# Kernel optimization log

Hardware: AMD Instinct MI355X
Metric: run time of the kernel (lower is better)

Reference implementation:

```python
import jax, jax.numpy as jnp
import numpy as np

B, N, DIN, H, D = 16, 1024, 128, 4, 32  # batch, n_agents, input_dim, heads, head_dim
NEG = -9e15


def setup_inputs() -> dict:
    key = jax.random.key(0)
    k1, k2, k3, k4 = jax.random.split(key, 4)
    x = jax.random.normal(k1, (B, N, DIN), jnp.float32)
    adj = jax.random.randint(k2, (B, N, N), 0, 2, jnp.int32)
    # params (xavier-ish scale)
    W = jax.random.normal(k3, (DIN, H * D), jnp.float32) * np.float32(1.0 / np.sqrt(DIN))
    b = jnp.zeros((H * D,), jnp.float32)
    a = jax.random.normal(k4, (2 * D, 1), jnp.float32) * np.float32(0.1)
    return {"x": x, "adj": adj, "W": W, "b": b, "a": a}


def reference(x, adj, W, b, a):
    Bb, Nn, _ = x.shape
    h = (x @ W + b).reshape(Bb, Nn, H, D)              # [B,N,H,D]
    # GAT trick: concat([h_i,h_j]) @ a == h_i@a[:D] + h_j@a[D:]
    a_i, a_j = a[:D, 0], a[D:, 0]
    e_i = jnp.einsum('bnhd,d->bnh', h, a_i)
    e_j = jnp.einsum('bnhd,d->bnh', h, a_j)
    e = e_i[:, :, None, :] + e_j[:, None, :, :]        # [B,N,N,H]
    e = jnp.where(e > 0, e, 0.2 * e)                   # LeakyReLU(0.2)
    e = jnp.where(adj[..., None] > 0, e, NEG)          # adjacency mask
    attn = jax.nn.softmax(e, axis=2)                   # softmax over neighbors j
    out = jnp.einsum('bijh,bjhd->bihd', attn, h)       # per-head aggregation
    return out.reshape(Bb, Nn, H * D)                  # concat heads
```

## Files before the change

kernel.cpp:

```cpp
#include <hip/hip_runtime.h>
#include <hip/hip_bf16.h>

#define Bdim 16
#define Ndim 1024
#define Hh   4
#define HDc  128
#define L2E  1.4426950408889634f

typedef float  float4v  __attribute__((ext_vector_type(4)));
typedef int    int4v    __attribute__((ext_vector_type(4)));
typedef short  short8   __attribute__((ext_vector_type(8)));
typedef unsigned short ushort4v __attribute__((ext_vector_type(4)));

__device__ __forceinline__ unsigned short bf16_rne(float f) {
    unsigned u = __float_as_uint(f);
    u = u + 0x7FFFu + ((u >> 16) & 1u);
    return (unsigned short)(u >> 16);
}

__device__ __forceinline__ void gl_lds16(const void* g, void* l) {
    __builtin_amdgcn_global_load_lds(
        (const __attribute__((address_space(1))) unsigned int*)g,
        (__attribute__((address_space(3))) unsigned int*)l, 16, 0, 0);
}

__global__ __launch_bounds__(256) void split_w_kernel(
    const float* __restrict__ W, const float* __restrict__ bias,
    const float* __restrict__ a,
    unsigned short* __restrict__ WTh, unsigned short* __restrict__ WTl,
    float* __restrict__ bias2)
{
    const int t = threadIdx.x, blk = blockIdx.x;
    if (blk < 16) {
        int r  = blk * 8 + (t >> 5);
        int k0 = (t & 31) * 4;
        #pragma unroll
        for (int j = 0; j < 4; ++j) {
            float f = W[(size_t)(k0 + j) * HDc + r];
            unsigned short hi = bf16_rne(f);
            WTh[r * 128 + k0 + j] = hi;
            WTl[r * 128 + k0 + j] = bf16_rne(f - __uint_as_float((unsigned)hi << 16));
        }
    } else {
        #pragma unroll
        for (int rep = 0; rep < 2; ++rep) {
            int task = t + rep * 256;
            int row = task >> 2, hh = task & 3;
            float si = 0.f, sj = 0.f;
            #pragma unroll
            for (int d4 = 0; d4 < 8; ++d4) {
                float4v wv = *(const float4v*)(W + (size_t)row * HDc + hh * 32 + d4 * 4);
                float4v av = *(const float4v*)(a + d4 * 4);
                float4v bv = *(const float4v*)(a + 32 + d4 * 4);
                #pragma unroll
                for (int kk = 0; kk < 4; ++kk) {
                    si = fmaf(wv[kk], av[kk], si);
                    sj = fmaf(wv[kk], bv[kk], sj);
                }
            }
            float vi = si * L2E, vj = sj * L2E;
            unsigned short hi = bf16_rne(vi);
            WTh[(128 + hh) * 128 + row] = hi;
            WTl[(128 + hh) * 128 + row] = bf16_rne(vi - __uint_as_float((unsigned)hi << 16));
            unsigned short hj = bf16_rne(vj);
            WTh[(132 + hh) * 128 + row] = hj;
            WTl[(132 + hh) * 128 + row] = bf16_rne(vj - __uint_as_float((unsigned)hj << 16));
        }
        #pragma unroll
        for (int rp = 0; rp < 4; ++rp) {
            int idx = t + rp * 256;
            WTh[136 * 128 + idx] = 0;
            WTl[136 * 128 + idx] = 0;
        }
        if (t < 128) {
            bias2[t] = bias[t];
        } else if (t < 136) {
            int z = t - 128;
            const float* av = (z < 4) ? a : a + 32;
            int hh = z & 3;
            float s = 0.f;
            for (int d = 0; d < 32; ++d) s = fmaf(bias[hh * 32 + d], av[d], s);
            bias2[128 + z] = s * L2E;
        } else if (t < 144) {
            bias2[t] = 0.f;
        }
    }
}

__global__ __launch_bounds__(256, 1) void proj_kernel(
    const float* __restrict__ x,
    const unsigned short* __restrict__ WTg_h, const unsigned short* __restrict__ WTg_l,
    const float* __restrict__ bias2,
    unsigned short* __restrict__ hTh, float* __restrict__ eiT, float* __restrict__ ejT)
{
    __shared__ __align__(16) unsigned char smem[106496];
    char* xls  = (char*)smem;
    char* wtls = (char*)smem + 32768;

    const int t = threadIdx.x, lane = t & 63, w = t >> 6;
    const int l16 = lane & 15, q = lane >> 4;
    const int nb = blockIdx.x * 64;
    const int b = nb >> 10, nloc = nb & 1023;

    {
        const char* gx = (const char*)(x + (size_t)nb * 128);
        int rh = lane >> 5, m = lane & 31;
        #pragma unroll
        for (int d = 0; d < 8; ++d) {
            int r = w * 16 + d * 2 + rh;
            int mg = m ^ (r & 7);
            gl_lds16(gx + (size_t)r * 512 + mg * 16, xls + (size_t)w * 8192 + d * 1024);
        }
    }
    {
        int rh = lane >> 4, m = lane & 15;
        #pragma unroll
        for (int d = 0; d < 18; ++d) {
            int n = w * 18 + d;
            if (n < 36) {
                int r = n * 4 + rh;
                gl_lds16((const char*)WTg_h + (size_t)r * 256 + (m ^ (r & 15)) * 16,
                         wtls + (size_t)n * 1024);
            } else {
                int r = (n - 36) * 4 + rh;
                gl_lds16((const char*)WTg_l + (size_t)r * 256 + (m ^ (r & 15)) * 16,
                         wtls + (size_t)n * 1024);
            }
        }
    }
    __syncthreads();

    float4v C[9];
    #pragma unroll
    for (int nt = 0; nt < 9; ++nt) C[nt] = (float4v){0.f, 0.f, 0.f, 0.f};

    #pragma unroll
    for (int ks = 0; ks < 4; ++ks) {
        short8 Ah, Al;
        {
            int r = w * 16 + l16;
            int c0 = (ks * 8 + q * 2) ^ (l16 & 7);
            int c1 = (ks * 8 + q * 2 + 1) ^ (l16 & 7);
            float4v x0 = *(const float4v*)(xls + (size_t)r * 512 + c0 * 16);
            float4v x1 = *(const float4v*)(xls + (size_t)r * 512 + c1 * 16);
            #pragma unroll
            for (int e = 0; e < 8; ++e) {
                float f = (e < 4) ? x0[e] : x1[e - 4];
                unsigned short hi = bf16_rne(f);
                Ah[e] = (short)hi;
                Al[e] = (short)bf16_rne(f - __uint_as_float((unsigned)hi << 16));
            }
        }
        #pragma unroll
        for (int nt = 0; nt < 9; ++nt) {
            const char* wb = wtls + (size_t)(nt * 16 + l16) * 256 + ((ks * 4 + q) ^ l16) * 16;
            short8 Bh = *(const short8*)wb;
            short8 Bl = *(const short8*)(wb + 36864);
            C[nt] = __builtin_amdgcn_mfma_f32_16x16x32_bf16(Ah, Bh, C[nt], 0, 0, 0);
            C[nt] = __builtin_amdgcn_mfma_f32_16x16x32_bf16(Ah, Bl, C[nt], 0, 0, 0);
            C[nt] = __builtin_amdgcn_mfma_f32_16x16x32_bf16(Al, Bh, C[nt], 0, 0, 0);
        }
    }

    {
        int node = nloc + w * 16 + q * 4;
        #pragma unroll
        for (int nt = 0; nt < 8; ++nt) {
            int col = nt * 16 + l16;
            float bv = bias2[col];
            ushort4v h4;
            #pragma unroll
            for (int r = 0; r < 4; ++r) h4[r] = bf16_rne(C[nt][r] + bv);
            *(ushort4v*)(hTh + (size_t)(b * HDc + col) * Ndim + node) = h4;
        }
        float bv = bias2[128 + l16];
        float4v v = {C[8][0] + bv, C[8][1] + bv, C[8][2] + bv, C[8][3] + bv};
        if (l16 < 4)
            *(float4v*)(eiT + (size_t)(b * Hh + l16) * Ndim + node) = v;
        else if (l16 < 8)
            *(float4v*)(ejT + (size_t)(b * Hh + (l16 - 4)) * Ndim + node) = v;
    }
}

__global__ __launch_bounds__(256, 4) void gat_kernel(
    const int* __restrict__ adj, const unsigned short* __restrict__ hTh,
    const float* __restrict__ eiT, const float* __restrict__ ejT,
    float* __restrict__ out)
{
    __shared__ __align__(16) unsigned char smem[26624];
    unsigned int* pkl = (unsigned int*)smem;
    char* rings = (char*)smem + 2048;

    const int t = threadIdx.x, lane = t & 63, w = t >> 6;
    const int L = blockIdx.x;
    const int b = (L & 7) + 8 * ((L >> 3) & 1);
    const int ibase = (L >> 4) * 16;
    const int i = lane & 15, q = lane >> 4;

    {
        const int m = lane & 31, rh = lane >> 5;
        const int r0 = w * 4 + rh;
        const int r1 = w * 4 + 2 + rh;
        const int4v* s0 = (const int4v*)(adj + ((size_t)(b * Ndim + ibase + r0)) * Ndim + m * 32);
        const int4v* s1 = (const int4v*)(adj + ((size_t)(b * Ndim + ibase + r1)) * Ndim + m * 32);
        int4v va[8], vb[8];
        #pragma unroll
        for (int u = 0; u < 8; ++u) va[u] = __builtin_nontemporal_load(s0 + u);
        #pragma unroll
        for (int u = 0; u < 8; ++u) vb[u] = __builtin_nontemporal_load(s1 + u);
        unsigned wa = 0, wb_ = 0;
        #pragma unroll
        for (int u = 0; u < 8; ++u) {
            unsigned na = (unsigned)(va[u][0] | (va[u][1] << 1) | (va[u][2] << 2) | (va[u][3] << 3));
            unsigned nb_ = (unsigned)(vb[u][0] | (vb[u][1] << 1) | (vb[u][2] << 2) | (vb[u][3] << 3));
            wa  |= na  << (4 * u);
            wb_ |= nb_ << (4 * u);
        }
        pkl[r0 * 32 + ((m + r0) & 31)] = wa;
        pkl[r1 * 32 + ((m + r1) & 31)] = wb_;
    }
    const float my_ei = eiT[(size_t)(b * Hh + w) * Ndim + ibase + i];
    __syncthreads();

    const char* gh = (const char*)(hTh + (size_t)(b * HDc + w * 32) * Ndim);
    const float* ej_p = ejT + (size_t)(b * Hh + w) * Ndim + q * 8;
    const size_t lane_g = (size_t)(lane >> 2) * 2048 + (lane & 3) * 16;
    char* ringw = rings + w * 6144;

#define ISSUE(JT, SLOT) {                                                   \
    char* lb_ = ringw + (SLOT) * 2048;                                      \
    gl_lds16(gh + (size_t)(JT) * 64 + lane_g,         lb_);                 \
    gl_lds16(gh + 32768 + (size_t)(JT) * 64 + lane_g, lb_ + 1024); }

    ISSUE(0, 0); ISSUE(1, 1);

    float4v C0 = {0.f, 0.f, 0.f, 0.f};
    float4v C1 = {0.f, 0.f, 0.f, 0.f};
    float den_a = 0.f, den_b = 0.f;

    int slot_c = 0;
    for (int jt = 0; jt < 32; ++jt) {
        int ji = jt + 2; if (ji > 31) ji = 31;
        int slot_i = slot_c + 2; if (slot_i >= 3) slot_i -= 3;
        ISSUE(ji, slot_i);
        asm volatile("s_waitcnt vmcnt(4)" ::: "memory");

        const char* lb = ringw + slot_c * 2048;
        short8 Bh0 = *(const short8*)(lb + i * 64 + q * 16);
        short8 Bh1 = *(const short8*)(lb + 1024 + i * 64 + q * 16);
        float4v e0 = *(const float4v*)(ej_p + jt * 32);
        float4v e1 = *(const float4v*)(ej_p + jt * 32 + 4);

        unsigned bits = (pkl[i * 32 + ((jt + i) & 31)] >> (q * 8)) & 0xffu;
        float p[8];
        #pragma unroll
        for (int k = 0; k < 8; ++k) {
            float ev = (k < 4) ? e0[k] : e1[k - 4];
            float e = my_ei + ev;
            float sL = fmaxf(e, 0.2f * e);
            float pe = ((bits >> k) & 1u) ? __builtin_amdgcn_exp2f(sL) : 0.f;
            if (k & 1) den_b += pe; else den_a += pe;
            p[k] = pe;
        }
        union { __hip_bfloat162 h2[4]; short8 s8; } A;
        #pragma unroll
        for (int k2 = 0; k2 < 4; ++k2)
            A.h2[k2] = __float22bfloat162_rn(make_float2(p[2 * k2], p[2 * k2 + 1]));
        C0 = __builtin_amdgcn_mfma_f32_16x16x32_bf16(A.s8, Bh0, C0, 0, 0, 0);
        C1 = __builtin_amdgcn_mfma_f32_16x16x32_bf16(A.s8, Bh1, C1, 0, 0, 0);
        slot_c = (slot_c == 2) ? 0 : slot_c + 1;
    }
#undef ISSUE

    float den = den_a + den_b;
    den += __shfl_xor(den, 16);
    den += __shfl_xor(den, 32);

    float* outp = out + ((size_t)(b * Ndim + ibase)) * HDc + w * 32 + i;
    #pragma unroll
    for (int reg = 0; reg < 4; ++reg) {
        int row = q * 4 + reg;
        float rd = 1.0f / __shfl(den, row, 64);
        outp[(size_t)row * HDc]      = C0[reg] * rd;
        outp[(size_t)row * HDc + 16] = C1[reg] * rd;
    }
}

extern "C" void kernel_launch(void* const* d_in, const int* in_sizes, int n_in,
                              void* d_out, int out_size, void* d_ws, size_t ws_size,
                              hipStream_t stream) {
    const float* x    = (const float*)d_in[0];
    const int*   adj  = (const int*)d_in[1];
    const float* W    = (const float*)d_in[2];
    const float* bias = (const float*)d_in[3];
    const float* a    = (const float*)d_in[4];
    float* out = (float*)d_out;

    unsigned short* hTh = (unsigned short*)d_ws;
    float* eiT = (float*)(hTh + (size_t)Bdim * HDc * Ndim);
    float* ejT = eiT + (size_t)Bdim * Hh * Ndim;
    unsigned short* WTh = (unsigned short*)(ejT + (size_t)Bdim * Hh * Ndim);
    unsigned short* WTl = WTh + 144 * 128;
    float* bias2 = (float*)(WTl + 144 * 128);

    split_w_kernel<<<dim3(17), dim3(256), 0, stream>>>(W, bias, a, WTh, WTl, bias2);
    proj_kernel<<<dim3(256), dim3(256), 0, stream>>>(
        x, WTh, WTl, bias2, hTh, eiT, ejT);
    gat_kernel<<<dim3(1024), dim3(256), 0, stream>>>(
        adj, hTh, eiT, ejT, out);
}
```

Before: 169.0 us.

## Stage h and ej in larger swizzled LDS chunks with block-wide sync

Replaces the per-wave 3-slot ring of 2KB async loads with a chunked scheme: each of 8 chunks loads 128 columns of h (swizzled to avoid bank conflicts) plus the ej values into LDS, then four MFMA steps run on that chunk. The aim is larger, more coalesced transfers (256B contiguous per row), and ej now comes from LDS instead of direct global loads. The cost is two block-wide barriers per chunk with no overlap between loading and compute, and LDS use rises from 26KB to 36KB, which may limit occupancy.

```diff
diff --git a/kernel.cpp b/kernel.cpp
--- a/kernel.cpp
+++ b/kernel.cpp
@@ -187,9 +187,10 @@
     const float* __restrict__ eiT, const float* __restrict__ ejT,
     float* __restrict__ out)
 {
-    __shared__ __align__(16) unsigned char smem[26624];
+    __shared__ __align__(16) unsigned char smem[36864];
     unsigned int* pkl = (unsigned int*)smem;
-    char* rings = (char*)smem + 2048;
+    float* ejlf = (float*)(smem + 2048);
+    char* hts = (char*)smem + 4096;
 
     const int t = threadIdx.x, lane = t & 63, w = t >> 6;
     const int L = blockIdx.x;
@@ -211,7 +212,7 @@
         unsigned wa = 0, wb_ = 0;
         #pragma unroll
         for (int u = 0; u < 8; ++u) {
-            unsigned na = (unsigned)(va[u][0] | (va[u][1] << 1) | (va[u][2] << 2) | (va[u][3] << 3));
+            unsigned na  = (unsigned)(va[u][0] | (va[u][1] << 1) | (va[u][2] << 2) | (va[u][3] << 3));
             unsigned nb_ = (unsigned)(vb[u][0] | (vb[u][1] << 1) | (vb[u][2] << 2) | (vb[u][3] << 3));
             wa  |= na  << (4 * u);
             wb_ |= nb_ << (4 * u);
@@ -220,57 +221,64 @@
         pkl[r1 * 32 + ((m + r1) & 31)] = wb_;
     }
     const float my_ei = eiT[(size_t)(b * Hh + w) * Ndim + ibase + i];
-    __syncthreads();
-
-    const char* gh = (const char*)(hTh + (size_t)(b * HDc + w * 32) * Ndim);
-    const float* ej_p = ejT + (size_t)(b * Hh + w) * Ndim + q * 8;
-    const size_t lane_g = (size_t)(lane >> 2) * 2048 + (lane & 3) * 16;
-    char* ringw = rings + w * 6144;
-
-#define ISSUE(JT, SLOT) {                                                   \
-    char* lb_ = ringw + (SLOT) * 2048;                                      \
-    gl_lds16(gh + (size_t)(JT) * 64 + lane_g,         lb_);                 \
-    gl_lds16(gh + 32768 + (size_t)(JT) * 64 + lane_g, lb_ + 1024); }
-
-    ISSUE(0, 0); ISSUE(1, 1);
+
+    const char* ghh = (const char*)(hTh + (size_t)(b * HDc + w * 32) * Ndim);
+    const char* gej = (const char*)(ejT + (size_t)(b * Hh) * Ndim);
+    const int drow = lane >> 4;
+    const int p16  = lane & 15;
+    const char* hrow0 = hts + (w * 32 + i) * 256;
+    const char* hrow1 = hts + (w * 32 + 16 + i) * 256;
+    const float* ejw = ejlf + w * 128;
 
     float4v C0 = {0.f, 0.f, 0.f, 0.f};
     float4v C1 = {0.f, 0.f, 0.f, 0.f};
     float den_a = 0.f, den_b = 0.f;
-
-    int slot_c = 0;
-    for (int jt = 0; jt < 32; ++jt) {
-        int ji = jt + 2; if (ji > 31) ji = 31;
-        int slot_i = slot_c + 2; if (slot_i >= 3) slot_i -= 3;
-        ISSUE(ji, slot_i);
-        asm volatile("s_waitcnt vmcnt(4)" ::: "memory");
-
-        const char* lb = ringw + slot_c * 2048;
-        short8 Bh0 = *(const short8*)(lb + i * 64 + q * 16);
-        short8 Bh1 = *(const short8*)(lb + 1024 + i * 64 + q * 16);
-        float4v e0 = *(const float4v*)(ej_p + jt * 32);
-        float4v e1 = *(const float4v*)(ej_p + jt * 32 + 4);
-
-        unsigned bits = (pkl[i * 32 + ((jt + i) & 31)] >> (q * 8)) & 0xffu;
-        float p[8];
-        #pragma unroll
-        for (int k = 0; k < 8; ++k) {
-            float ev = (k < 4) ? e0[k] : e1[k - 4];
-            float e = my_ei + ev;
-            float sL = fmaxf(e, 0.2f * e);
-            float pe = ((bits >> k) & 1u) ? __builtin_amdgcn_exp2f(sL) : 0.f;
-            if (k & 1) den_b += pe; else den_a += pe;
-            p[k] = pe;
-        }
-        union { __hip_bfloat162 h2[4]; short8 s8; } A;
-        #pragma unroll
-        for (int k2 = 0; k2 < 4; ++k2)
-            A.h2[k2] = __float22bfloat162_rn(make_float2(p[2 * k2], p[2 * k2 + 1]));
-        C0 = __builtin_amdgcn_mfma_f32_16x16x32_bf16(A.s8, Bh0, C0, 0, 0, 0);
-        C1 = __builtin_amdgcn_mfma_f32_16x16x32_bf16(A.s8, Bh1, C1, 0, 0, 0);
-        slot_c = (slot_c == 2) ? 0 : slot_c + 1;
-    }
-#undef ISSUE
+    __syncthreads();
+
+    for (int ch = 0; ch < 8; ++ch) {
+        if (ch) __syncthreads();
+        #pragma unroll
+        for (int u = 0; u < 8; ++u) {
+            int d = u * 4 + drow;
+            int c = p16 ^ (d & 15);
+            gl_lds16(ghh + (size_t)d * 2048 + ch * 256 + c * 16,
+                     hts + (w * 32 + u * 4) * 256);
+        }
+        if (w < 2) {
+            int hh = w * 2 + (lane >> 5);
+            gl_lds16(gej + (size_t)hh * 4096 + ch * 512 + (lane & 31) * 16,
+                     (char*)ejlf + w * 1024);
+        }
+        __syncthreads();
+
+        #pragma unroll
+        for (int jtl = 0; jtl < 4; ++jtl) {
+            const int jt = ch * 4 + jtl;
+            const int pc = ((jtl * 4 + q) ^ i) * 16;
+            short8 Bh0 = *(const short8*)(hrow0 + pc);
+            short8 Bh1 = *(const short8*)(hrow1 + pc);
+            float4v e0 = *(const float4v*)(ejw + jtl * 32 + q * 8);
+            float4v e1 = *(const float4v*)(ejw + jtl * 32 + q * 8 + 4);
+            unsigned bits = (pkl[i * 32 + ((jt + i) & 31)] >> (q * 8)) & 0xffu;
+
+            float p[8];
+            #pragma unroll
+            for (int k = 0; k < 8; ++k) {
+                float ev = (k < 4) ? e0[k] : e1[k - 4];
+                float e = my_ei + ev;
+                float sL = fmaxf(e, 0.2f * e);
+                float pe = ((bits >> k) & 1u) ? __builtin_amdgcn_exp2f(sL) : 0.f;
+                if (k & 1) den_b += pe; else den_a += pe;
+                p[k] = pe;
+            }
+            union { __hip_bfloat162 h2[4]; short8 s8; } A;
+            #pragma unroll
+            for (int k2 = 0; k2 < 4; ++k2)
+                A.h2[k2] = __float22bfloat162_rn(make_float2(p[2 * k2], p[2 * k2 + 1]));
+            C0 = __builtin_amdgcn_mfma_f32_16x16x32_bf16(A.s8, Bh0, C0, 0, 0, 0);
+            C1 = __builtin_amdgcn_mfma_f32_16x16x32_bf16(A.s8, Bh1, C1, 0, 0, 0);
+        }
+    }
 
     float den = den_a + den_b;
     den += __shfl_xor(den, 16);
```

After: 166.3 us. About the same (-1.6%).
